# Optimization experiments

Measured on AMD Instinct MI355X. Metric: run time of the kernel, lower is better.

Reference implementation:

```python
import jax, jax.numpy as jnp
import numpy as np

B, C, H, W = 4, 256, 64, 64
CH = C // 2  # inner channels


def setup_inputs() -> dict:
    key = jax.random.key(0)
    ks = jax.random.split(key, 9)
    s = 1.0 / np.sqrt(C)
    so = 1.0 / np.sqrt(CH)
    return {
        "x": jax.random.normal(ks[0], (B, C, H, W), dtype=jnp.float32),
        "teta_w": jax.random.uniform(ks[1], (CH, C), jnp.float32, -s, s),
        "teta_b": jax.random.uniform(ks[2], (CH,), jnp.float32, -s, s),
        "fi_w": jax.random.uniform(ks[3], (CH, C), jnp.float32, -s, s),
        "fi_b": jax.random.uniform(ks[4], (CH,), jnp.float32, -s, s),
        "gi_w": jax.random.uniform(ks[5], (CH, C), jnp.float32, -s, s),
        "gi_b": jax.random.uniform(ks[6], (CH,), jnp.float32, -s, s),
        "out_w": jax.random.uniform(ks[7], (C, CH), jnp.float32, -so, so),
        "out_b": jax.random.uniform(ks[8], (C,), jnp.float32, -so, so),
    }


def _conv1x1(x, w, b):
    # x: (B, Cin, H, W), w: (Cout, Cin) -> (B, Cout, H, W)
    return jnp.einsum('bchw,oc->bohw', x, w) + b[None, :, None, None]


def reference(x, teta_w, teta_b, fi_w, fi_b, gi_w, gi_b, out_w, out_b):
    b, c, h, w = x.shape
    n = h * w
    ch = teta_w.shape[0]
    # NOTE: original uses .view (reshape), NOT transpose, to get (B, N, Ch)
    x1 = _conv1x1(x, teta_w, teta_b).reshape(b, ch, n).reshape(b, n, ch)
    x2 = _conv1x1(x, fi_w, fi_b).reshape(b, ch, n)            # (B, Ch, N)
    x3 = _conv1x1(x, gi_w, gi_b).reshape(b, ch, n).reshape(b, n, ch)
    # softmax over dim=1 (rows), as in the original
    attn = jax.nn.softmax(jnp.matmul(x1, x2), axis=1)          # (B, N, N)
    y = jnp.matmul(attn, x3)                                   # (B, N, Ch)
    y = jnp.swapaxes(y, 1, 2).reshape(b, ch, h, w)
    return x + _conv1x1(y, out_w, out_b)
```

## Files before the change

### kernel.cpp

```cpp
#include <hip/hip_runtime.h>
#include <hip/hip_bf16.h>

#define BB 4
#define CC 256
#define CHH 128
#define NN 4096
#define KSHIFT 12.0f

typedef __attribute__((ext_vector_type(8))) short bf16x8;
typedef __attribute__((ext_vector_type(4))) float f32x4;

__device__ __forceinline__ float to_f(float v) { return v; }
__device__ __forceinline__ float to_f(__hip_bfloat16 v) { return __bfloat162float(v); }
__device__ __forceinline__ void st_f(float* p, float v) { *p = v; }
__device__ __forceinline__ void st_f(__hip_bfloat16* p, float v) { *p = __float2bfloat16(v); }
__device__ __forceinline__ unsigned short f2bf(float f) {
    __hip_bfloat16 h = __float2bfloat16(f);
    unsigned short u;
    __builtin_memcpy(&u, &h, 2);
    return u;
}
__device__ __forceinline__ bf16x8 ldb8(const unsigned short* p) { return *(const bf16x8*)p; }

__device__ __forceinline__ void gload_lds16(const unsigned short* g, unsigned short* l) {
    __builtin_amdgcn_global_load_lds(
        (const __attribute__((address_space(1))) unsigned int*)g,
        (__attribute__((address_space(3))) unsigned int*)l, 16, 0, 0);
}

__global__ void detect_kernel(const void* __restrict__ tb, int* __restrict__ flag) {
    if (threadIdx.x == 0) {
        const __hip_bfloat16* p = (const __hip_bfloat16*)tb;
        int big = 0, zeros = 0;
        for (int i = 0; i < 128; ++i) {
            float v = __bfloat162float(p[i]);
            if (!(fabsf(v) <= 0.5f)) big = 1;
            if ((i & 1) == 0 && v == 0.0f) zeros++;
        }
        *flag = (big || zeros >= 32) ? 1 : 0;
    }
}

template <typename T>
__device__ __forceinline__ void prep_body(const T* tw, const T* fw, const T* gw, const T* ow,
                                          const T* tb2, const T* fb, const T* gb, const T* ob,
                                          unsigned short* Wb, unsigned short* OWb,
                                          float* Bf, float* OBf) {
    int idx = blockIdx.x * 256 + threadIdx.x;
    if (idx < 98304) {
        int cv = idx >> 15, rem = idx & 32767;
        const T* src = cv == 0 ? tw : (cv == 1 ? fw : gw);
        Wb[idx] = f2bf(to_f(src[rem]));
    } else if (idx < 131072) {
        OWb[idx - 98304] = f2bf(to_f(ow[idx - 98304]));
    } else if (idx < 131456) {
        int r = idx - 131072;
        int cv = r >> 7, j = r & 127;
        const T* src = cv == 0 ? tb2 : (cv == 1 ? fb : gb);
        Bf[r] = to_f(src[j]);
    } else if (idx < 131712) {
        OBf[idx - 131456] = to_f(ob[idx - 131456]);
    }
}

__global__ void prep_kernel(const void* tw, const void* fw, const void* gw, const void* ow,
                            const void* tb2, const void* fb, const void* gb, const void* ob,
                            const int* __restrict__ flag,
                            unsigned short* Wb, unsigned short* OWb, float* Bf, float* OBf) {
    if (*flag)
        prep_body<float>((const float*)tw, (const float*)fw, (const float*)gw, (const float*)ow,
                         (const float*)tb2, (const float*)fb, (const float*)gb, (const float*)ob,
                         Wb, OWb, Bf, OBf);
    else
        prep_body<__hip_bfloat16>((const __hip_bfloat16*)tw, (const __hip_bfloat16*)fw,
                                  (const __hip_bfloat16*)gw, (const __hip_bfloat16*)ow,
                                  (const __hip_bfloat16*)tb2, (const __hip_bfloat16*)fb,
                                  (const __hip_bfloat16*)gb, (const __hip_bfloat16*)ob,
                                  Wb, OWb, Bf, OBf);
}

template <typename T>
__device__ __forceinline__ void xtrans_body(const T* __restrict__ x, unsigned short* __restrict__ xt) {
    int b = blockIdx.z;
    const T* in = x + (size_t)b * CC * NN;
    unsigned short* out = xt + (size_t)b * NN * CC;
    int p0 = blockIdx.x * 64, c0 = blockIdx.y * 64;
    __shared__ unsigned short t[64][68];
    int flat = threadIdx.x;
#pragma unroll
    for (int tt = 0; tt < 16; ++tt) {
        int id = flat + tt * 256;
        int rr = id >> 6, cc = id & 63;
        t[cc][rr] = f2bf(to_f(in[(size_t)(c0 + rr) * NN + p0 + cc]));
    }
    __syncthreads();
#pragma unroll
    for (int tt = 0; tt < 16; ++tt) {
        int id = flat + tt * 256;
        int pp = id >> 6, jj = id & 63;
        out[(size_t)(p0 + pp) * CC + c0 + jj] = t[pp][jj];
    }
}

__launch_bounds__(256)
__global__ void xtrans_kernel(const void* x, const int* __restrict__ flag,
                              unsigned short* __restrict__ xt) {
    if (*flag) xtrans_body<float>((const float*)x, xt);
    else       xtrans_body<__hip_bfloat16>((const __hip_bfloat16*)x, xt);
}

__launch_bounds__(256)
__global__ void conv3_mfma_kernel(const unsigned short* __restrict__ xt,
                                  const unsigned short* __restrict__ Wb,
                                  const float* __restrict__ Bf,
                                  unsigned short* __restrict__ T1b,
                                  unsigned short* __restrict__ T2b,
                                  unsigned short* __restrict__ T3b) {
    int b = blockIdx.y;
    int p0 = blockIdx.x * 16;
    int flat = threadIdx.x;
    int w = flat >> 6, lane = flat & 63, m = lane & 15, quad = lane >> 4;
    const unsigned short* xrow = xt + ((size_t)b * NN + p0 + m) * CC;
    bf16x8 xf[8];
#pragma unroll
    for (int kc = 0; kc < 8; ++kc)
        xf[kc] = ldb8(&xrow[kc * 32 + quad * 8]);
    unsigned short* outs[3] = {T1b + (size_t)b * CHH * NN,
                               T2b + (size_t)b * CHH * NN,
                               T3b + (size_t)b * CHH * NN};
#pragma unroll
    for (int q = 0; q < 6; ++q) {
        int t = w * 6 + q;
        int cv = t >> 3, ot = t & 7;
        int o0 = ot * 16;
        const unsigned short* wrow = Wb + ((size_t)cv * CHH + o0 + m) * CC;
        f32x4 acc = {0.f, 0.f, 0.f, 0.f};
#pragma unroll
        for (int kc = 0; kc < 8; ++kc) {
            bf16x8 wf = ldb8(&wrow[kc * 32 + quad * 8]);
            acc = __builtin_amdgcn_mfma_f32_16x16x32_bf16(wf, xf[kc], acc, 0, 0, 0);
        }
#pragma unroll
        for (int r = 0; r < 4; ++r) {
            int o = o0 + quad * 4 + r;
            outs[cv][(size_t)o * NN + p0 + m] = f2bf(acc[r] + Bf[cv * CHH + o]);
        }
    }
}

__launch_bounds__(256)
__global__ void transpose_kernel(const unsigned short* __restrict__ in,
                                 unsigned short* __restrict__ out, int R, int C) {
    int bz = blockIdx.z;
    in  += (size_t)bz * R * C;
    out += (size_t)bz * R * C;
    int c0 = blockIdx.x * 64, r0 = blockIdx.y * 64;
    __shared__ unsigned short t[64][68];
    int flat = threadIdx.x;
#pragma unroll
    for (int tt = 0; tt < 16; ++tt) {
        int id = flat + tt * 256;
        int r = id >> 6, c = id & 63;
        t[c][r] = in[(size_t)(r0 + r) * C + c0 + c];
    }
    __syncthreads();
#pragma unroll
    for (int tt = 0; tt < 16; ++tt) {
        int id = flat + tt * 256;
        int c = id >> 6, r = id & 63;
        out[(size_t)(c0 + c) * R + r0 + r] = t[c][r];
    }
}

__launch_bounds__(256)
__global__ void stats_mfma_kernel(const unsigned short* __restrict__ T1b,
                                  const unsigned short* __restrict__ T2t,
                                  float* __restrict__ Lpart) {
    int blk = blockIdx.x;
    int b = (blk & 7) >> 1;
    int rest = (blk >> 3) * 2 + (blk & 1);
    int strip = rest >> 3, iq = rest & 7;
    int ibase = iq * 512;
    int flat = threadIdx.x;
    int w = flat >> 6, lane = flat & 63, m = lane & 15, quad = lane >> 4;
    const unsigned short* A  = T1b + (size_t)b * CHH * NN;
    const unsigned short* Bt = T2t + (size_t)b * CHH * NN;
    __shared__ unsigned short th[64 * 128];

    int u0w = strip * 128 + w * 32;
    bf16x8 bfr[2][4];
#pragma unroll
    for (int g = 0; g < 2; ++g)
#pragma unroll
        for (int kc = 0; kc < 4; ++kc)
            bfr[g][kc] = ldb8(&Bt[(size_t)(u0w + g * 16 + m) * CHH + kc * 32 + quad * 8]);

    float csum[2] = {0.f, 0.f};
    for (int t = 0; t < 8; ++t) {
        int i0t = ibase + t * 64;
        __syncthreads();
#pragma unroll
        for (int i = 0; i < 4; ++i) {
            int sl = i * 256 + flat;
            int r = sl >> 4, ch = sl & 15;
            int c = ch ^ (r & 7);
            gload_lds16(&A[(size_t)(i0t + r) * CHH + c * 8], &th[sl * 8]);
        }
        __syncthreads();
#pragma unroll
        for (int s = 0; s < 4; ++s) {
            int irow = s * 16 + m;
            bf16x8 af[4];
#pragma unroll
            for (int kc = 0; kc < 4; ++kc) {
                int ch = (kc * 4 + quad) ^ (irow & 7);
                af[kc] = *(const bf16x8*)&th[irow * 128 + ch * 8];
            }
#pragma unroll
            for (int g = 0; g < 2; ++g) {
                f32x4 acc = {0.f, 0.f, 0.f, 0.f};
#pragma unroll
                for (int kc = 0; kc < 4; ++kc)
                    acc = __builtin_amdgcn_mfma_f32_16x16x32_bf16(af[kc], bfr[g][kc], acc, 0, 0, 0);
#pragma unroll
                for (int r = 0; r < 4; ++r)
                    csum[g] += __expf(acc[r] - KSHIFT);
            }
        }
    }
#pragma unroll
    for (int g = 0; g < 2; ++g) {
        csum[g] += __shfl_xor(csum[g], 16, 64);
        csum[g] += __shfl_xor(csum[g], 32, 64);
        if (lane < 16)
            Lpart[((size_t)iq * BB + b) * NN + u0w + g * 16 + m] = csum[g];
    }
}

__global__ void lmerge_kernel(const float* __restrict__ Lpart, float* __restrict__ LL) {
    int idx = blockIdx.x * 256 + threadIdx.x;
    int b = idx >> 12, u = idx & 4095;
    float s = 0.f;
#pragma unroll
    for (int c = 0; c < 8; ++c)
        s += Lpart[((size_t)c * BB + b) * NN + u];
    LL[idx] = logf(s) + KSHIFT;
}

__launch_bounds__(256)
__global__ void attn_mfma_kernel(const unsigned short* __restrict__ T1b,
                                 const unsigned short* __restrict__ T2t,
                                 const unsigned short* __restrict__ X3t,
                                 const float* __restrict__ LL,
                                 unsigned short* __restrict__ Yp0,
                                 unsigned short* __restrict__ Yp1,
                                 unsigned short* __restrict__ Yp2,
                                 unsigned short* __restrict__ Yp3) {
    int blk = blockIdx.x;
    int b = (blk & 7) >> 1;
    int rest = (blk >> 3) * 2 + (blk & 1);
    int it = rest >> 2, uc = rest & 3;
    int i0 = it * 64;
    unsigned short* Yp = uc == 0 ? Yp0 : (uc == 1 ? Yp1 : (uc == 2 ? Yp2 : Yp3));
    int flat = threadIdx.x;
    int w = flat >> 6, lane = flat & 63, m = lane & 15, quad = lane >> 4;
    const unsigned short* A  = T1b + (size_t)b * CHH * NN;
    const unsigned short* Bt = T2t + (size_t)b * CHH * NN;
    const unsigned short* X3 = X3t + (size_t)b * CHH * NN;
    const float* LLb = LL + (size_t)b * NN;

    __shared__ unsigned short bt[64 * 128];
    __shared__ unsigned short x3[128 * 64];
    __shared__ unsigned short pT[4][16][40];

    int iw = i0 + w * 16;
    bf16x8 ath[4];
#pragma unroll
    for (int kc = 0; kc < 4; ++kc)
        ath[kc] = ldb8(&A[(size_t)(iw + m) * CHH + kc * 32 + quad * 8]);
    f32x4 yacc[8];
#pragma unroll
    for (int js = 0; js < 8; ++js) yacc[js] = (f32x4){0.f, 0.f, 0.f, 0.f};

    int ubeg = uc * 1024, uend = ubeg + 1024;
    for (int u0 = ubeg; u0 < uend; u0 += 64) {
        __syncthreads();
#pragma unroll
        for (int i = 0; i < 4; ++i) {
            int sl = i * 256 + flat;
            int u = sl >> 4, ch = sl & 15;
            int c = ch ^ (u & 7);
            gload_lds16(&Bt[(size_t)(u0 + u) * CHH + c * 8], &bt[sl * 8]);
        }
#pragma unroll
        for (int i = 0; i < 4; ++i) {
            int sl = i * 256 + flat;
            int j = sl >> 3, ch = sl & 7;
            int c = ch ^ (j & 7);
            gload_lds16(&X3[(size_t)j * NN + u0 + c * 8], &x3[sl * 8]);
        }
        __syncthreads();
#pragma unroll
        for (int h = 0; h < 2; ++h) {
#pragma unroll
            for (int su = 0; su < 2; ++su) {
                int u = (h * 2 + su) * 16 + m;
                f32x4 acc = {0.f, 0.f, 0.f, 0.f};
#pragma unroll
                for (int kc = 0; kc < 4; ++kc) {
                    int ch = (kc * 4 + quad) ^ (u & 7);
                    bf16x8 bf = *(const bf16x8*)&bt[u * 128 + ch * 8];
                    acc = __builtin_amdgcn_mfma_f32_16x16x32_bf16(ath[kc], bf, acc, 0, 0, 0);
                }
                float ll = LLb[u0 + u];
#pragma unroll
                for (int r = 0; r < 4; ++r)
                    pT[w][quad * 4 + r][su * 16 + m] = f2bf(__expf(acc[r] - ll));
            }
            bf16x8 pa = *(const bf16x8*)&pT[w][m][quad * 8];
#pragma unroll
            for (int js = 0; js < 8; ++js) {
                int j = js * 16 + m;
                int ch = (h * 4 + quad) ^ (j & 7);
                bf16x8 xb = *(const bf16x8*)&x3[j * 64 + ch * 8];
                yacc[js] = __builtin_amdgcn_mfma_f32_16x16x32_bf16(pa, xb, yacc[js], 0, 0, 0);
            }
        }
    }
#pragma unroll
    for (int js = 0; js < 8; ++js)
#pragma unroll
        for (int r = 0; r < 4; ++r)
            Yp[((size_t)b * NN + iw + quad * 4 + r) * CHH + js * 16 + m] = f2bf(yacc[js][r]);
}

template <typename T>
__device__ __forceinline__ void outconv_body(const T* __restrict__ x,
                                             const unsigned short* __restrict__ Yp0,
                                             const unsigned short* __restrict__ Yp1,
                                             const unsigned short* __restrict__ Yp2,
                                             const unsigned short* __restrict__ Yp3,
                                             const unsigned short* __restrict__ OWb,
                                             const float* __restrict__ OBf,
                                             T* __restrict__ out) {
    int b = blockIdx.y;
    int p0 = blockIdx.x * 16;
    int flat = threadIdx.x;
    int w = flat >> 6, lane = flat & 63, m = lane & 15, quad = lane >> 4;
    size_t yoff = ((size_t)b * NN + p0 + m) * CHH;
    const unsigned short* yrows[4] = {Yp0 + yoff, Yp1 + yoff, Yp2 + yoff, Yp3 + yoff};
    bf16x8 yf[4][4];
#pragma unroll
    for (int pz = 0; pz < 4; ++pz)
#pragma unroll
        for (int kc = 0; kc < 4; ++kc)
            yf[pz][kc] = ldb8(&yrows[pz][kc * 32 + quad * 8]);
#pragma unroll
    for (int q = 0; q < 4; ++q) {
        int o0 = (w * 4 + q) * 16;
        const unsigned short* wrow = OWb + (size_t)(o0 + m) * CHH;
        f32x4 acc = {0.f, 0.f, 0.f, 0.f};
#pragma unroll
        for (int kc = 0; kc < 4; ++kc) {
            bf16x8 aw = ldb8(&wrow[kc * 32 + quad * 8]);
#pragma unroll
            for (int pz = 0; pz < 4; ++pz)
                acc = __builtin_amdgcn_mfma_f32_16x16x32_bf16(aw, yf[pz][kc], acc, 0, 0, 0);
        }
#pragma unroll
        for (int r = 0; r < 4; ++r) {
            int co = o0 + quad * 4 + r;
            size_t oi = ((size_t)b * CC + co) * NN + p0 + m;
            st_f(&out[oi], acc[r] + OBf[co] + to_f(x[oi]));
        }
    }
}

__launch_bounds__(256)
__global__ void outconv_mfma_kernel(const void* x,
                                    const unsigned short* __restrict__ Yp0,
                                    const unsigned short* __restrict__ Yp1,
                                    const unsigned short* __restrict__ Yp2,
                                    const unsigned short* __restrict__ Yp3,
                                    const unsigned short* __restrict__ OWb,
                                    const float* __restrict__ OBf,
                                    const int* __restrict__ flag, void* out) {
    if (*flag)
        outconv_body<float>((const float*)x, Yp0, Yp1, Yp2, Yp3, OWb, OBf, (float*)out);
    else
        outconv_body<__hip_bfloat16>((const __hip_bfloat16*)x, Yp0, Yp1, Yp2, Yp3, OWb, OBf,
                                     (__hip_bfloat16*)out);
}

extern "C" void kernel_launch(void* const* d_in, const int* in_sizes, int n_in,
                              void* d_out, int out_size, void* d_ws, size_t ws_size,
                              hipStream_t stream) {
    const void* x  = d_in[0];
    const void* tw = d_in[1];
    const void* tb = d_in[2];
    const void* fw = d_in[3];
    const void* fb = d_in[4];
    const void* gw = d_in[5];
    const void* gb = d_in[6];
    const void* ow = d_in[7];
    const void* ob = d_in[8];

    const size_t TE = (size_t)BB * CHH * NN;
    unsigned short* T1b = (unsigned short*)d_ws;
    unsigned short* T2b = T1b + TE;
    unsigned short* T3b = T2b + TE;
    unsigned short* xt  = T3b + TE;
    unsigned short* T2t = xt;
    unsigned short* X3t = xt + TE;
    unsigned short* Yp0 = T2b;
    unsigned short* Yp1 = T3b;
    unsigned short* Yp2 = xt + 2 * TE;
    unsigned short* Yp3 = Yp2 + TE;
    unsigned short* Wb  = Yp3 + TE;
    unsigned short* OWb = Wb + 98304;
    float* Bf    = (float*)(OWb + 32768);
    float* OBf   = Bf + 384;
    float* Lpart = OBf + 256;
    float* LLb   = Lpart + 131072;
    int*   Flag  = (int*)(LLb + 16384);

    detect_kernel<<<1, 64, 0, stream>>>(tb, Flag);
    prep_kernel<<<dim3(515), 256, 0, stream>>>(tw, fw, gw, ow, tb, fb, gb, ob,
                                               Flag, Wb, OWb, Bf, OBf);
    xtrans_kernel<<<dim3(NN / 64, CC / 64, BB), 256, 0, stream>>>(x, Flag, xt);
    conv3_mfma_kernel<<<dim3(NN / 16, BB), 256, 0, stream>>>(xt, Wb, Bf, T1b, T2b, T3b);
    transpose_kernel<<<dim3(NN / 64, CHH / 64, BB), 256, 0, stream>>>(T2b, T2t, CHH, NN);
    transpose_kernel<<<dim3(CHH / 64, NN / 64, BB), 256, 0, stream>>>(T3b, X3t, NN, CHH);
    stats_mfma_kernel<<<dim3(1024), 256, 0, stream>>>(T1b, T2t, Lpart);
    lmerge_kernel<<<dim3(BB * NN / 256), 256, 0, stream>>>(Lpart, LLb);
    attn_mfma_kernel<<<dim3(1024), 256, 0, stream>>>(T1b, T2t, X3t, LLb, Yp0, Yp1, Yp2, Yp3);
    outconv_mfma_kernel<<<dim3(NN / 16, BB), 256, 0, stream>>>(x, Yp0, Yp1, Yp2, Yp3,
                                                               OWb, OBf, Flag, d_out);
}
```

Measured before the change: 231.6 us.

## Fuse T2 transpose into conv, merge lmerge into attention, double attention row tile

The conv kernel now writes the fi projection directly in transposed layout through a lane shuffle, which removes one transpose kernel. The log-sum merge is folded into the attention kernel, which computes its 1024 normalisers into shared memory, so the separate lmerge launch goes away. Each attention block now handles 128 query rows (two 16-row groups per wave) so every staged bt/x3 tile is reused twice, and the grid is halved to 512 blocks. In exchange, each wave holds more accumulator registers (occupancy risk), the grid has fewer blocks, and the Lpart reduction is recomputed redundantly per block.

```diff
diff --git a/kernel.cpp b/kernel.cpp
--- a/kernel.cpp
+++ b/kernel.cpp
@@ -114,7 +114,7 @@
                                   const unsigned short* __restrict__ Wb,
                                   const float* __restrict__ Bf,
                                   unsigned short* __restrict__ T1b,
-                                  unsigned short* __restrict__ T2b,
+                                  unsigned short* __restrict__ T2t,
                                   unsigned short* __restrict__ T3b) {
     int b = blockIdx.y;
     int p0 = blockIdx.x * 16;
@@ -125,9 +125,9 @@
 #pragma unroll
     for (int kc = 0; kc < 8; ++kc)
         xf[kc] = ldb8(&xrow[kc * 32 + quad * 8]);
-    unsigned short* outs[3] = {T1b + (size_t)b * CHH * NN,
-                               T2b + (size_t)b * CHH * NN,
-                               T3b + (size_t)b * CHH * NN};
+    unsigned short* t1  = T1b + (size_t)b * CHH * NN;
+    unsigned short* t2t = T2t + (size_t)b * CHH * NN;
+    unsigned short* t3  = T3b + (size_t)b * CHH * NN;
 #pragma unroll
     for (int q = 0; q < 6; ++q) {
         int t = w * 6 + q;
@@ -140,10 +140,25 @@
             bf16x8 wf = ldb8(&wrow[kc * 32 + quad * 8]);
             acc = __builtin_amdgcn_mfma_f32_16x16x32_bf16(wf, xf[kc], acc, 0, 0, 0);
         }
-#pragma unroll
-        for (int r = 0; r < 4; ++r) {
-            int o = o0 + quad * 4 + r;
-            outs[cv][(size_t)o * NN + p0 + m] = f2bf(acc[r] + Bf[cv * CHH + o]);
+        unsigned short hv[4];
+#pragma unroll
+        for (int r = 0; r < 4; ++r)
+            hv[r] = f2bf(acc[r] + Bf[cv * CHH + o0 + quad * 4 + r]);
+        if (cv == 1) {
+            unsigned int lo = (unsigned int)hv[0] | ((unsigned int)hv[1] << 16);
+            unsigned int hi = (unsigned int)hv[2] | ((unsigned int)hv[3] << 16);
+            int src = (lane & 3) * 16 + (lane >> 2);
+            unsigned int tlo = (unsigned int)__shfl((int)lo, src, 64);
+            unsigned int thi = (unsigned int)__shfl((int)hi, src, 64);
+            unsigned int* dst = (unsigned int*)&t2t[(size_t)(p0 + (lane >> 2)) * CHH +
+                                                    o0 + (lane & 3) * 4];
+            dst[0] = tlo;
+            dst[1] = thi;
+        } else {
+            unsigned short* outp = (cv == 0) ? t1 : t3;
+#pragma unroll
+            for (int r = 0; r < 4; ++r)
+                outp[(size_t)(o0 + quad * 4 + r) * NN + p0 + m] = hv[r];
         }
     }
 }
@@ -237,21 +252,11 @@
     }
 }
 
-__global__ void lmerge_kernel(const float* __restrict__ Lpart, float* __restrict__ LL) {
-    int idx = blockIdx.x * 256 + threadIdx.x;
-    int b = idx >> 12, u = idx & 4095;
-    float s = 0.f;
-#pragma unroll
-    for (int c = 0; c < 8; ++c)
-        s += Lpart[((size_t)c * BB + b) * NN + u];
-    LL[idx] = logf(s) + KSHIFT;
-}
-
 __launch_bounds__(256)
 __global__ void attn_mfma_kernel(const unsigned short* __restrict__ T1b,
                                  const unsigned short* __restrict__ T2t,
                                  const unsigned short* __restrict__ X3t,
-                                 const float* __restrict__ LL,
+                                 const float* __restrict__ Lpart,
                                  unsigned short* __restrict__ Yp0,
                                  unsigned short* __restrict__ Yp1,
                                  unsigned short* __restrict__ Yp2,
@@ -260,30 +265,45 @@
     int b = (blk & 7) >> 1;
     int rest = (blk >> 3) * 2 + (blk & 1);
     int it = rest >> 2, uc = rest & 3;
-    int i0 = it * 64;
+    int i0 = it * 128;
     unsigned short* Yp = uc == 0 ? Yp0 : (uc == 1 ? Yp1 : (uc == 2 ? Yp2 : Yp3));
     int flat = threadIdx.x;
     int w = flat >> 6, lane = flat & 63, m = lane & 15, quad = lane >> 4;
     const unsigned short* A  = T1b + (size_t)b * CHH * NN;
     const unsigned short* Bt = T2t + (size_t)b * CHH * NN;
     const unsigned short* X3 = X3t + (size_t)b * CHH * NN;
-    const float* LLb = LL + (size_t)b * NN;
 
     __shared__ unsigned short bt[64 * 128];
     __shared__ unsigned short x3[128 * 64];
-    __shared__ unsigned short pT[4][16][40];
-
-    int iw = i0 + w * 16;
-    bf16x8 ath[4];
-#pragma unroll
-    for (int kc = 0; kc < 4; ++kc)
-        ath[kc] = ldb8(&A[(size_t)(iw + m) * CHH + kc * 32 + quad * 8]);
-    f32x4 yacc[8];
-#pragma unroll
-    for (int js = 0; js < 8; ++js) yacc[js] = (f32x4){0.f, 0.f, 0.f, 0.f};
-
-    int ubeg = uc * 1024, uend = ubeg + 1024;
-    for (int u0 = ubeg; u0 < uend; u0 += 64) {
+    __shared__ unsigned short pT[4][2][16][40];
+    __shared__ float llh[1024];
+
+    int ubeg = uc * 1024;
+#pragma unroll
+    for (int k = 0; k < 4; ++k) {
+        int idx = k * 256 + flat;
+        int u = ubeg + idx;
+        float s = 0.f;
+#pragma unroll
+        for (int c = 0; c < 8; ++c)
+            s += Lpart[((size_t)c * BB + b) * NN + u];
+        llh[idx] = logf(s) + KSHIFT;
+    }
+
+    int iw = i0 + w * 32;
+    bf16x8 ath[2][4];
+#pragma unroll
+    for (int g = 0; g < 2; ++g)
+#pragma unroll
+        for (int kc = 0; kc < 4; ++kc)
+            ath[g][kc] = ldb8(&A[(size_t)(iw + g * 16 + m) * CHH + kc * 32 + quad * 8]);
+    f32x4 yacc[2][8];
+#pragma unroll
+    for (int g = 0; g < 2; ++g)
+#pragma unroll
+        for (int js = 0; js < 8; ++js) yacc[g][js] = (f32x4){0.f, 0.f, 0.f, 0.f};
+
+    for (int u0 = ubeg; u0 < ubeg + 1024; u0 += 64) {
         __syncthreads();
 #pragma unroll
         for (int i = 0; i < 4; ++i) {
@@ -304,34 +324,42 @@
         for (int h = 0; h < 2; ++h) {
 #pragma unroll
             for (int su = 0; su < 2; ++su) {
-                int u = (h * 2 + su) * 16 + m;
-                f32x4 acc = {0.f, 0.f, 0.f, 0.f};
+                int u = h * 32 + su * 16 + m;
+                f32x4 a0 = {0.f, 0.f, 0.f, 0.f}, a1 = {0.f, 0.f, 0.f, 0.f};
 #pragma unroll
                 for (int kc = 0; kc < 4; ++kc) {
                     int ch = (kc * 4 + quad) ^ (u & 7);
                     bf16x8 bf = *(const bf16x8*)&bt[u * 128 + ch * 8];
-                    acc = __builtin_amdgcn_mfma_f32_16x16x32_bf16(ath[kc], bf, acc, 0, 0, 0);
+                    a0 = __builtin_amdgcn_mfma_f32_16x16x32_bf16(ath[0][kc], bf, a0, 0, 0, 0);
+                    a1 = __builtin_amdgcn_mfma_f32_16x16x32_bf16(ath[1][kc], bf, a1, 0, 0, 0);
                 }
-                float ll = LLb[u0 + u];
-#pragma unroll
-                for (int r = 0; r < 4; ++r)
-                    pT[w][quad * 4 + r][su * 16 + m] = f2bf(__expf(acc[r] - ll));
+                float ll = llh[u0 - ubeg + u];
+#pragma unroll
+                for (int r = 0; r < 4; ++r) {
+                    pT[w][0][quad * 4 + r][su * 16 + m] = f2bf(__expf(a0[r] - ll));
+                    pT[w][1][quad * 4 + r][su * 16 + m] = f2bf(__expf(a1[r] - ll));
+                }
             }
-            bf16x8 pa = *(const bf16x8*)&pT[w][m][quad * 8];
+            bf16x8 pa0 = *(const bf16x8*)&pT[w][0][m][quad * 8];
+            bf16x8 pa1 = *(const bf16x8*)&pT[w][1][m][quad * 8];
 #pragma unroll
             for (int js = 0; js < 8; ++js) {
                 int j = js * 16 + m;
                 int ch = (h * 4 + quad) ^ (j & 7);
                 bf16x8 xb = *(const bf16x8*)&x3[j * 64 + ch * 8];
-                yacc[js] = __builtin_amdgcn_mfma_f32_16x16x32_bf16(pa, xb, yacc[js], 0, 0, 0);
+                yacc[0][js] = __builtin_amdgcn_mfma_f32_16x16x32_bf16(pa0, xb, yacc[0][js], 0, 0, 0);
+                yacc[1][js] = __builtin_amdgcn_mfma_f32_16x16x32_bf16(pa1, xb, yacc[1][js], 0, 0, 0);
             }
         }
     }
 #pragma unroll
-    for (int js = 0; js < 8; ++js)
-#pragma unroll
-        for (int r = 0; r < 4; ++r)
-            Yp[((size_t)b * NN + iw + quad * 4 + r) * CHH + js * 16 + m] = f2bf(yacc[js][r]);
+    for (int g = 0; g < 2; ++g)
+#pragma unroll
+        for (int js = 0; js < 8; ++js)
+#pragma unroll
+            for (int r = 0; r < 4; ++r)
+                Yp[((size_t)b * NN + iw + g * 16 + quad * 4 + r) * CHH + js * 16 + m] =
+                    f2bf(yacc[g][js][r]);
 }
 
 template <typename T>
@@ -407,33 +435,29 @@
 
     const size_t TE = (size_t)BB * CHH * NN;
     unsigned short* T1b = (unsigned short*)d_ws;
-    unsigned short* T2b = T1b + TE;
-    unsigned short* T3b = T2b + TE;
+    unsigned short* T2t = T1b + TE;
+    unsigned short* X3t = T2t + TE;
+    unsigned short* T3b = X3t + TE;
     unsigned short* xt  = T3b + TE;
-    unsigned short* T2t = xt;
-    unsigned short* X3t = xt + TE;
-    unsigned short* Yp0 = T2b;
-    unsigned short* Yp1 = T3b;
-    unsigned short* Yp2 = xt + 2 * TE;
-    unsigned short* Yp3 = Yp2 + TE;
+    unsigned short* Yp0 = xt;
+    unsigned short* Yp1 = xt + TE;
+    unsigned short* Yp2 = T3b;
+    unsigned short* Yp3 = xt + 2 * TE;
     unsigned short* Wb  = Yp3 + TE;
     unsigned short* OWb = Wb + 98304;
     float* Bf    = (float*)(OWb + 32768);
     float* OBf   = Bf + 384;
     float* Lpart = OBf + 256;
-    float* LLb   = Lpart + 131072;
-    int*   Flag  = (int*)(LLb + 16384);
+    int*   Flag  = (int*)(Lpart + 131072);
 
     detect_kernel<<<1, 64, 0, stream>>>(tb, Flag);
     prep_kernel<<<dim3(515), 256, 0, stream>>>(tw, fw, gw, ow, tb, fb, gb, ob,
                                                Flag, Wb, OWb, Bf, OBf);
     xtrans_kernel<<<dim3(NN / 64, CC / 64, BB), 256, 0, stream>>>(x, Flag, xt);
-    conv3_mfma_kernel<<<dim3(NN / 16, BB), 256, 0, stream>>>(xt, Wb, Bf, T1b, T2b, T3b);
-    transpose_kernel<<<dim3(NN / 64, CHH / 64, BB), 256, 0, stream>>>(T2b, T2t, CHH, NN);
+    conv3_mfma_kernel<<<dim3(NN / 16, BB), 256, 0, stream>>>(xt, Wb, Bf, T1b, T2t, T3b);
     transpose_kernel<<<dim3(CHH / 64, NN / 64, BB), 256, 0, stream>>>(T3b, X3t, NN, CHH);
     stats_mfma_kernel<<<dim3(1024), 256, 0, stream>>>(T1b, T2t, Lpart);
-    lmerge_kernel<<<dim3(BB * NN / 256), 256, 0, stream>>>(Lpart, LLb);
-    attn_mfma_kernel<<<dim3(1024), 256, 0, stream>>>(T1b, T2t, X3t, LLb, Yp0, Yp1, Yp2, Yp3);
+    attn_mfma_kernel<<<dim3(512), 256, 0, stream>>>(T1b, T2t, X3t, Lpart, Yp0, Yp1, Yp2, Yp3);
     outconv_mfma_kernel<<<dim3(NN / 16, BB), 256, 0, stream>>>(x, Yp0, Yp1, Yp2, Yp3,
                                                                OWb, OBf, Flag, d_out);
 }
```

Result: faster. 213.9 us (-7.6%).
